# Optimization experiments

Measured on AMD Instinct MI355X. Metric: run time of the kernel, lower is better.

The kernel has to match this reference:

```python
import jax, jax.numpy as jnp
import numpy as np

N = 20000   # nodes per type per hop
E = 200000  # edges per relation per hop
H = 512     # node_feature_hid_len
FU = 512    # raw user feature len
FI = 256    # raw item feature len
NUM_RES = 2
NUM_DNN = 2


def setup_inputs() -> dict:
    key = jax.random.key(0)
    ks = iter(jax.random.split(key, 64))
    p = lambda shape: jax.random.normal(next(ks), shape, dtype=jnp.float32) * 0.05
    inp = {}
    # features per hop per type
    for h in range(3):
        inp[f'feat_user_h{h}'] = jax.random.normal(next(ks), (N, FU), dtype=jnp.float32)
        inp[f'feat_item_h{h}'] = jax.random.normal(next(ks), (N, FI), dtype=jnp.float32)
    del inp['feat_user_h2_']; 


def _unused():
    pass

# rebuild setup_inputs cleanly (above stub replaced)

def setup_inputs() -> dict:
    key = jax.random.key(0)
    ks = iter(jax.random.split(key, 64))
    p = lambda shape: jax.random.normal(next(ks), shape, dtype=jnp.float32) * 0.05
    inp = {}
    for h in range(3):
        inp[f'feat_user_h{h}'] = jax.random.normal(next(ks), (N, FU), dtype=jnp.float32)
        inp[f'feat_item_h{h}'] = jax.random.normal(next(ks), (N, FI), dtype=jnp.float32)
    for name in ('edges_UI_h0', 'edges_IU_h0', 'edges_UI_h1', 'edges_IU_h1'):
        inp[name] = jax.random.randint(next(ks), (2, E), 0, N, dtype=jnp.int32)
    # per-node-type input transforms
    inp['W_user'] = p((FU, H)); inp['b_user'] = jnp.zeros((H,), jnp.float32)
    inp['W_item'] = p((FI, H)); inp['b_item'] = jnp.zeros((H,), jnp.float32)
    # per-relation GATConv params, stacked over 2 relations [UI, IU]
    inp['gat_feat_W'] = p((2, H, H)); inp['gat_feat_b'] = jnp.zeros((2, H), jnp.float32)
    inp['gat_att_w'] = p((2, 2 * H)); inp['gat_att_b'] = jnp.zeros((2,), jnp.float32)
    inp['gat_bias'] = jnp.zeros((2, H), jnp.float32)
    # Res_DNN params
    inp['prep_W'] = p((H, H)); inp['prep_b'] = jnp.zeros((H,), jnp.float32)
    inp['dnn_W'] = p((NUM_RES, NUM_DNN, H, H)); inp['dnn_b'] = jnp.zeros((NUM_RES, NUM_DNN, H), jnp.float32)
    inp['dnn_ln_g'] = jnp.ones((NUM_RES, NUM_DNN, H), jnp.float32); inp['dnn_ln_b'] = jnp.zeros((NUM_RES, NUM_DNN, H), jnp.float32)
    inp['res_ln_g'] = jnp.ones((NUM_RES, H), jnp.float32); inp['res_ln_b'] = jnp.zeros((NUM_RES, H), jnp.float32)
    inp['cls_W'] = p((H, 1)); inp['cls_b'] = jnp.zeros((1,), jnp.float32)
    return inp


def _ln(x, g, b, eps=1e-5):
    mu = jnp.mean(x, axis=-1, keepdims=True)
    var = jnp.mean((x - mu) ** 2, axis=-1, keepdims=True)
    return (x - mu) * jax.lax.rsqrt(var + eps) * g + b


def _gat(head_h, tail_h, edges, fW, fb, aw, ab, bias):
    # GATConv: feat_linear on both sides, tanh edge attention, per-source-row
    # sparse softmax, scatter-weighted sum of transformed tail features.
    s = head_h @ fW + fb            # [Nh, H]
    t = tail_h @ fW + fb            # [Nt, H]
    src, tgt = edges[0], edges[1]
    # att(cat([s_e, t_e])) split into per-node scores (same math as concat @ aw)
    e = jnp.tanh((s @ aw[:H])[src] + (t @ aw[H:])[tgt] + ab)  # [E]
    nh = head_h.shape[0]
    m = jax.ops.segment_max(e, src, num_segments=nh)
    ex = jnp.exp(e - m[src])
    den = jax.ops.segment_sum(ex, src, num_segments=nh)
    alpha = ex / den[src]
    hp = jax.ops.segment_sum(alpha[:, None] * t[tgt], src, num_segments=nh)
    return hp + bias


def _forward(feat_user_h0, feat_item_h0, feat_user_h1, feat_item_h1,
             feat_user_h2, feat_item_h2,
             W_user, b_user, W_item, b_item,
             gat_feat_W, gat_feat_b, gat_att_w, gat_att_b, gat_bias,
             prep_W, prep_b, dnn_W, dnn_b, dnn_ln_g, dnn_ln_b,
             res_ln_g, res_ln_b, cls_W, cls_b,
             edges_UI_h0, edges_IU_h0, edges_UI_h1, edges_IU_h1):
    def gat(r, head, tail, edges):
        return _gat(head, tail, edges, gat_feat_W[r], gat_feat_b[r],
                    gat_att_w[r], gat_att_b[r], gat_bias[r])
    # hop 2 (deepest): transformed source features
    su = feat_user_h2 @ W_user + b_user
    si = feat_item_h2 @ W_item + b_item
    # hop 1
    hu = feat_user_h1 @ W_user + b_user
    hi = feat_item_h1 @ W_item + b_item
    su_new = (hu + gat(0, hu, si, edges_UI_h1)) * 0.5  # mean of [self, UI agg]
    si_new = (hi + gat(1, hi, su, edges_IU_h1)) * 0.5
    su, si = su_new, si_new
    # hop 0
    hu = feat_user_h0 @ W_user + b_user
    hi = feat_item_h0 @ W_item + b_item
    su_new = (hu + gat(0, hu, si, edges_UI_h0)) * 0.5
    su = su_new  # target node type = 'user' (first key)
    # Res_DNN head
    x = su @ prep_W + prep_b
    for r in range(NUM_RES):
        sc = x
        for d in range(NUM_DNN):
            x = _ln(jnp.tanh(x @ dnn_W[r, d] + dnn_b[r, d]), dnn_ln_g[r, d], dnn_ln_b[r, d])
        x = _ln(jnp.tanh(sc + x), res_ln_g[r], res_ln_b[r])
    return jax.nn.sigmoid(x @ cls_W + cls_b)  # [N, 1]


def reference(feat_user_h0, feat_item_h0, feat_user_h1, feat_item_h1,
              feat_user_h2, feat_item_h2,
              edges_UI_h0, edges_IU_h0, edges_UI_h1, edges_IU_h1,
              W_user, b_user, W_item, b_item,
              gat_feat_W, gat_feat_b, gat_att_w, gat_att_b, gat_bias,
              prep_W, prep_b, dnn_W, dnn_b, dnn_ln_g, dnn_ln_b,
              res_ln_g, res_ln_b, cls_W, cls_b):
    return _forward(feat_user_h0, feat_item_h0, feat_user_h1, feat_item_h1,
                    feat_user_h2, feat_item_h2,
                    W_user, b_user, W_item, b_item,
                    gat_feat_W, gat_feat_b, gat_att_w, gat_att_b, gat_bias,
                    prep_W, prep_b, dnn_W, dnn_b, dnn_ln_g, dnn_ln_b,
                    res_ln_g, res_ln_b, cls_W, cls_b,
                    edges_UI_h0, edges_IU_h0, edges_UI_h1, edges_IU_h1)
```

## Files before the change

### kernel.cpp

```cpp
#include <hip/hip_runtime.h>
#include <math.h>

#define NN 20000
#define NE 200000
#define HH 512

typedef __attribute__((ext_vector_type(8))) short short8v;
typedef __attribute__((ext_vector_type(4))) float f32x4;

__device__ inline short f2bf(float f) {
    union { float f; unsigned u; } v; v.f = f;
    unsigned r = (v.u + 0x7fffu + ((v.u >> 16) & 1u)) >> 16;
    return (short)r;
}
__device__ inline float bf2f(short s) {
    union { unsigned u; float f; } v;
    v.u = ((unsigned)(unsigned short)s) << 16;
    return v.f;
}

__device__ inline void gload_lds16(const void* g, void* l) {
    __builtin_amdgcn_global_load_lds(
        (const __attribute__((address_space(1))) void*)g,
        (__attribute__((address_space(3))) void*)l, 16, 0, 0);
}

__global__ __launch_bounds__(256)
void wtr_all(const float* __restrict__ Wu, const float* __restrict__ Wi,
             const float* __restrict__ gfW, const float* __restrict__ prW,
             const float* __restrict__ dW,
             short* __restrict__ WTu, short* __restrict__ WTi,
             short* __restrict__ WTg0, short* __restrict__ WTg1,
             short* __restrict__ WTpr, short* __restrict__ WTd)
{
    __shared__ float t[32][33];
    int z = blockIdx.z;
    const float* src; short* dst; int K;
    if (z == 0)      { src = Wu;  dst = WTu;  K = 512; }
    else if (z == 1) { src = Wi;  dst = WTi;  K = 256; }
    else if (z == 2) { src = gfW; dst = WTg0; K = 512; }
    else if (z == 3) { src = gfW + (size_t)512 * 512; dst = WTg1; K = 512; }
    else if (z == 4) { src = prW; dst = WTpr; K = 512; }
    else { src = dW + (size_t)(z - 5) * 512 * 512;
           dst = WTd + (size_t)(z - 5) * 512 * 512; K = 512; }
    int by = blockIdx.y * 32;
    if (by >= K) return;
    int bx = blockIdx.x * 32;
    int tx = threadIdx.x, ty = threadIdx.y;
    for (int i = ty; i < 32; i += 8)
        t[i][tx] = src[(size_t)(by + i) * 512 + bx + tx];
    __syncthreads();
    for (int i = ty; i < 32; i += 8)
        dst[(size_t)(bx + i) * K + by + tx] = f2bf(t[tx][i]);
}

__global__ __launch_bounds__(256)
void mfma_lin(const short* __restrict__ X, const short* __restrict__ WT,
              const float* __restrict__ bias, float* __restrict__ outF,
              short* __restrict__ outB, int M, int K,
              const short* __restrict__ rdH, const short* __restrict__ rdT,
              const float* __restrict__ rduv, const float* __restrict__ rds0,
              float* __restrict__ rdss, float* __restrict__ rdts, int rdN)
{
    __shared__ short8v pool[4096];

    const int tid = threadIdx.x;
    const int lane = tid & 63;
    const int w = tid >> 6;

    const int nby = (M + 127) >> 7;
    const int nwg = nby << 2;
    int id = blockIdx.x;

    if (id >= nwg) {
        int row = (id - nwg) * 4 + w;
        if (row >= rdN) return;
        short8v h = ((const short8v*)(rdH + (size_t)row * HH))[lane];
        short8v t = ((const short8v*)(rdT + (size_t)row * HH))[lane];
        const float4* up = (const float4*)rduv + lane * 2;
        const float4* vp = (const float4*)(rduv + HH) + lane * 2;
        float4 u0 = up[0], u1 = up[1], v0 = vp[0], v1 = vp[1];
        float a = bf2f(h[0])*u0.x + bf2f(h[1])*u0.y + bf2f(h[2])*u0.z + bf2f(h[3])*u0.w
                + bf2f(h[4])*u1.x + bf2f(h[5])*u1.y + bf2f(h[6])*u1.z + bf2f(h[7])*u1.w;
        float b = bf2f(t[0])*v0.x + bf2f(t[1])*v0.y + bf2f(t[2])*v0.z + bf2f(t[3])*v0.w
                + bf2f(t[4])*v1.x + bf2f(t[5])*v1.y + bf2f(t[6])*v1.z + bf2f(t[7])*v1.w;
#pragma unroll
        for (int m = 32; m >= 1; m >>= 1) {
            a += __shfl_xor(a, m);
            b += __shfl_xor(b, m);
        }
        if (lane == 0) { rdss[row] = a + rds0[0]; rdts[row] = b + rds0[1]; }
        return;
    }

    const int q = nwg >> 3, r = nwg & 7;
    int xcd = id & 7, wi = id >> 3;
    int wgid = (xcd < r ? xcd * (q + 1) : r * (q + 1) + (xcd - r) * q) + wi;
    const int col0 = (wgid & 3) * 128;
    const int row0 = (wgid >> 2) * 128;

    const int wr = (w >> 1) * 64;
    const int wc = (w & 1) * 64;

    const short* gsrc[8];
#pragma unroll
    for (int g = 0; g < 8; ++g) {
        int p = w * 512 + g * 64 + lane;
        if (p < 1024) {
            int row = p >> 3;
            int c = (p & 7) ^ (row & 7);
            int ga = row0 + row; if (ga >= M) ga = M - 1;
            gsrc[g] = X + (size_t)ga * K + c * 8;
        } else {
            int qq = p - 1024;
            int col = qq >> 3;
            int c = (qq & 7) ^ (col & 7);
            gsrc[g] = WT + (size_t)(col0 + col) * K + c * 8;
        }
    }

    int ar[2][4], br[2][4];
#pragma unroll
    for (int kk = 0; kk < 2; ++kk) {
#pragma unroll
        for (int i = 0; i < 4; ++i) {
            int rr = wr + i * 16 + (lane & 15);
            ar[kk][i] = rr * 8 + ((kk * 4 + (lane >> 4)) ^ (rr & 7));
            int nn = wc + i * 16 + (lane & 15);
            br[kk][i] = 1024 + nn * 8 + ((kk * 4 + (lane >> 4)) ^ (nn & 7));
        }
    }

    f32x4 acc[4][4];
#pragma unroll
    for (int i = 0; i < 4; ++i)
#pragma unroll
        for (int j = 0; j < 4; ++j)
            acc[i][j] = (f32x4){0.f, 0.f, 0.f, 0.f};

    auto stage = [&](int buf, int kk) {
        short8v* base = pool + buf * 2048 + w * 512;
#pragma unroll
        for (int g = 0; g < 8; ++g)
            gload_lds16(gsrc[g] + kk, base + g * 64);
    };

    const int nt = K >> 6;
    stage(0, 0);
    if (nt > 1) stage(1, 64);
    int cur = 0;
    for (int t = 0; t < nt; ++t) {
        if (t + 1 < nt) asm volatile("s_waitcnt vmcnt(8)" ::: "memory");
        else            asm volatile("s_waitcnt vmcnt(0)" ::: "memory");
        __builtin_amdgcn_s_barrier();
        const short8v* S = pool + cur * 2048;
#pragma unroll
        for (int kk = 0; kk < 2; ++kk) {
            short8v af[4], bf[4];
#pragma unroll
            for (int i = 0; i < 4; ++i) af[i] = S[ar[kk][i]];
#pragma unroll
            for (int j = 0; j < 4; ++j) bf[j] = S[br[kk][j]];
#pragma unroll
            for (int i = 0; i < 4; ++i)
#pragma unroll
                for (int j = 0; j < 4; ++j)
                    acc[i][j] = __builtin_amdgcn_mfma_f32_16x16x32_bf16(af[i], bf[j], acc[i][j], 0, 0, 0);
        }
        __builtin_amdgcn_s_barrier();
        if (t + 2 < nt) stage(cur, (t + 2) * 64);
        cur ^= 1;
    }

    float bj[4];
#pragma unroll
    for (int j = 0; j < 4; ++j)
        bj[j] = bias[col0 + wc + j * 16 + (lane & 15)];

    if (outF) {
#pragma unroll
        for (int i = 0; i < 4; ++i) {
#pragma unroll
            for (int rr = 0; rr < 4; ++rr) {
                int row = row0 + wr + i * 16 + (lane >> 4) * 4 + rr;
                if (row < M) {
                    float* op = outF + (size_t)row * HH + col0 + wc + (lane & 15);
#pragma unroll
                    for (int j = 0; j < 4; ++j) op[j * 16] = acc[i][j][rr] + bj[j];
                }
            }
        }
    }
    if (outB) {
        short* lt = (short*)pool;
#pragma unroll
        for (int i = 0; i < 4; ++i)
#pragma unroll
            for (int rr = 0; rr < 4; ++rr) {
                int lrow = wr + i * 16 + (lane >> 4) * 4 + rr;
#pragma unroll
                for (int j = 0; j < 4; ++j)
                    lt[lrow * 136 + wc + j * 16 + (lane & 15)] = f2bf(acc[i][j][rr] + bj[j]);
            }
        __syncthreads();
#pragma unroll
        for (int k = 0; k < 8; ++k) {
            int row = (tid >> 4) + 16 * k;
            int seg = tid & 15;
            int grow = row0 + row;
            if (grow < M) {
                short8v vv = *(short8v*)(lt + row * 136 + seg * 8);
                *(short8v*)(outB + (size_t)grow * HH + col0 + seg * 8) = vv;
            }
        }
    }
}

__global__ __launch_bounds__(256)
void mfma_linf(const float* __restrict__ XA, const float* __restrict__ XB2,
               int NA, const short* __restrict__ WT,
               const float* __restrict__ bias, short* __restrict__ outB,
               int M, int K)
{
    __shared__ short8v pool[3072];

    const int tid = threadIdx.x;
    const int lane = tid & 63;
    const int w = tid >> 6;

    const int nby = (M + 127) >> 7;
    const int nwg = nby << 2;
    const int q = nwg >> 3, r = nwg & 7;
    int id = blockIdx.x;
    int xcd = id & 7, wi = id >> 3;
    int wgid = (xcd < r ? xcd * (q + 1) : r * (q + 1) + (xcd - r) * q) + wi;
    const int col0 = (wgid & 3) * 128;
    const int row0 = (wgid >> 2) * 128;

    const int wr = (w >> 1) * 64;
    const int wc = (w & 1) * 64;
    const int kg = lane >> 4;

    const float* ga_[4];
#pragma unroll
    for (int g = 0; g < 4; ++g) {
        int p = w * 256 + g * 64 + lane;
        int row = p >> 3;
        int c = (p & 7) ^ (row & 7);
        int ga = row0 + row; if (ga >= M) ga = M - 1;
        const float* base = (ga < NA) ? XA + (size_t)ga * K
                                      : XB2 + (size_t)(ga - NA) * K;
        ga_[g] = base + c * 4;
    }
    const short* gb_[2];
#pragma unroll
    for (int g = 0; g < 2; ++g) {
        int p = w * 128 + g * 64 + lane;
        int col = p >> 2;
        int c = (p & 3) ^ ((col >> 1) & 3);
        gb_[g] = WT + (size_t)(col0 + col) * K + c * 8;
    }

    int arow[4], br_[4];
#pragma unroll
    for (int i = 0; i < 4; ++i) arow[i] = wr + i * 16 + (lane & 15);
#pragma unroll
    for (int j = 0; j < 4; ++j) {
        int nn = wc + j * 16 + (lane & 15);
        br_[j] = 1024 + nn * 4 + (kg ^ ((nn >> 1) & 3));
    }

    f32x4 acc[4][4];
#pragma unroll
    for (int i = 0; i < 4; ++i)
#pragma unroll
        for (int j = 0; j < 4; ++j)
            acc[i][j] = (f32x4){0.f, 0.f, 0.f, 0.f};

    auto stage = [&](int buf, int t) {
        short8v* base = pool + buf * 1536 + w * 256;
#pragma unroll
        for (int g = 0; g < 4; ++g)
            gload_lds16(ga_[g] + t * 32, base + g * 64);
        short8v* bb = pool + buf * 1536 + 1024 + w * 128;
#pragma unroll
        for (int g = 0; g < 2; ++g)
            gload_lds16(gb_[g] + t * 32, bb + g * 64);
    };

    const int nt = K >> 5;
    stage(0, 0);
    if (nt > 1) stage(1, 1);
    int cur = 0;
    for (int t = 0; t < nt; ++t) {
        if (t + 1 < nt) asm volatile("s_waitcnt vmcnt(6)" ::: "memory");
        else            asm volatile("s_waitcnt vmcnt(0)" ::: "memory");
        __builtin_amdgcn_s_barrier();
        const float4* Af = (const float4*)(pool + cur * 1536);
        const short8v* S = pool + cur * 1536;
        short8v af[4], bf[4];
#pragma unroll
        for (int i = 0; i < 4; ++i) {
            int rr = arow[i];
            int s = rr & 7;
            float4 lo = Af[rr * 8 + ((2 * kg)     ^ s)];
            float4 hi = Af[rr * 8 + ((2 * kg + 1) ^ s)];
            af[i][0] = f2bf(lo.x); af[i][1] = f2bf(lo.y);
            af[i][2] = f2bf(lo.z); af[i][3] = f2bf(lo.w);
            af[i][4] = f2bf(hi.x); af[i][5] = f2bf(hi.y);
            af[i][6] = f2bf(hi.z); af[i][7] = f2bf(hi.w);
        }
#pragma unroll
        for (int j = 0; j < 4; ++j) bf[j] = S[br_[j]];
#pragma unroll
        for (int i = 0; i < 4; ++i)
#pragma unroll
            for (int j = 0; j < 4; ++j)
                acc[i][j] = __builtin_amdgcn_mfma_f32_16x16x32_bf16(af[i], bf[j], acc[i][j], 0, 0, 0);
        __builtin_amdgcn_s_barrier();
        if (t + 2 < nt) stage(cur, t + 2);
        cur ^= 1;
    }

    float bj[4];
#pragma unroll
    for (int j = 0; j < 4; ++j)
        bj[j] = bias[col0 + wc + j * 16 + (lane & 15)];

    short* lt = (short*)pool;
#pragma unroll
    for (int i = 0; i < 4; ++i)
#pragma unroll
        for (int rr = 0; rr < 4; ++rr) {
            int lrow = wr + i * 16 + (lane >> 4) * 4 + rr;
#pragma unroll
            for (int j = 0; j < 4; ++j)
                lt[lrow * 136 + wc + j * 16 + (lane & 15)] = f2bf(acc[i][j][rr] + bj[j]);
        }
    __syncthreads();
#pragma unroll
    for (int k = 0; k < 8; ++k) {
        int row = (tid >> 4) + 16 * k;
        int seg = tid & 15;
        int grow = row0 + row;
        if (grow < M) {
            short8v vv = *(short8v*)(lt + row * 136 + seg * 8);
            *(short8v*)(outB + (size_t)grow * HH + col0 + seg * 8) = vv;
        }
    }
}

__global__ __launch_bounds__(256)
void gat_pre2(const float* __restrict__ gfW, const float* __restrict__ gfb,
              const float* __restrict__ gaw, float* __restrict__ uvall,
              float* __restrict__ s0t0all)
{
    int rrel = blockIdx.y;
    const float* fW = gfW + (size_t)rrel * HH * HH;
    const float* fb = gfb + rrel * HH;
    const float* aw = gaw + (size_t)rrel * 2 * HH;
    float* uv = uvall + rrel * 1024;
    float* s0t0 = s0t0all + rrel * 4;
    int row = blockIdx.x * 4 + (threadIdx.x >> 6);
    int lane = threadIdx.x & 63;
    const float4* ah = (const float4*)aw;
    const float4* at = (const float4*)(aw + HH);
    const float4* fp;
    if (row < 512)       fp = (const float4*)(fW + (size_t)row * HH);
    else if (row == 512) fp = (const float4*)fb;
    else return;
    float du = 0.f, dv = 0.f;
#pragma unroll
    for (int l = 0; l < 2; ++l) {
        int idx = lane * 2 + l;
        float4 f = fp[idx], a = ah[idx], b = at[idx];
        du += f.x*a.x + f.y*a.y + f.z*a.z + f.w*a.w;
        dv += f.x*b.x + f.y*b.y + f.z*b.z + f.w*b.w;
    }
#pragma unroll
    for (int m = 32; m >= 1; m >>= 1) {
        du += __shfl_xor(du, m);
        dv += __shfl_xor(dv, m);
    }
    if (lane == 0) {
        if (row < 512) { uv[row] = du; uv[512 + row] = dv; }
        else           { s0t0[0] = du; s0t0[1] = dv; }
    }
}

__global__ __launch_bounds__(256)
void count2_kernel(const int* __restrict__ s0, const int* __restrict__ s1,
                   int* __restrict__ c0, int* __restrict__ c1, int E)
{
    int i = blockIdx.x * blockDim.x + threadIdx.x;
    if (i < E) atomicAdd(&c0[s0[i]], 1);
    else if (i < 2 * E) atomicAdd(&c1[s1[i - E]], 1);
}

__global__ __launch_bounds__(1024)
void scan2_kernel(const int* __restrict__ c0, const int* __restrict__ c1,
                  int* __restrict__ o0, int* __restrict__ o1,
                  int* __restrict__ u0, int* __restrict__ u1, int n)
{
    const int* counts = blockIdx.x ? c1 : c0;
    int* offs = blockIdx.x ? o1 : o0;
    int* curs = blockIdx.x ? u1 : u0;
    __shared__ int part[1024];
    const int tid = threadIdx.x;
    const int CH = (n + 1023) / 1024;
    const int base = tid * CH;
    int s = 0;
    for (int i = 0; i < CH; ++i) {
        int idx = base + i;
        if (idx < n) s += counts[idx];
    }
    part[tid] = s;
    __syncthreads();
    for (int d = 1; d < 1024; d <<= 1) {
        int v = 0;
        if (tid >= d) v = part[tid - d];
        __syncthreads();
        if (tid >= d) part[tid] += v;
        __syncthreads();
    }
    int run = (tid == 0) ? 0 : part[tid - 1];
    for (int i = 0; i < CH; ++i) {
        int idx = base + i;
        if (idx < n) { offs[idx] = run; curs[idx] = run; run += counts[idx]; }
    }
    if (tid == 1023) offs[n] = run;
}

__global__ __launch_bounds__(256)
void fill_kernel(const int* __restrict__ src, const int* __restrict__ tgt,
                 const float* __restrict__ ss, const float* __restrict__ ts,
                 const float* __restrict__ ab_ptr, int* __restrict__ cursor,
                 int* __restrict__ tvals, float* __restrict__ wv,
                 int* __restrict__ eidx, int E)
{
    int i = blockIdx.x * blockDim.x + threadIdx.x;
    if (i >= E) return;
    int s = src[i], t = tgt[i];
    int pos = atomicAdd(&cursor[s], 1);
    tvals[pos] = t;
    wv[pos] = expf(tanhf(ss[s] + ts[t] + ab_ptr[0]));
    eidx[pos] = i;
}

__global__ __launch_bounds__(256)
void sortbkt_kernel(const int* __restrict__ offs, int* __restrict__ tvals,
                    float* __restrict__ wv, const int* __restrict__ eidx, int N)
{
    __shared__ int   lt[4][512];
    __shared__ float lw[4][512];
    int w = threadIdx.x >> 6, lane = threadIdx.x & 63;
    int s = blockIdx.x * 4 + w;
    if (s >= N) return;
    int beg = offs[s], end = offs[s + 1];
    int L = end - beg;
    if (L <= 1) return;
    if (L <= 64) {
        int e = 0x7fffffff, t = 0; float fw = 0.f;
        if (lane < L) { e = eidx[beg + lane]; t = tvals[beg + lane]; fw = wv[beg + lane]; }
        int r = 0;
        for (int k = 0; k < L; ++k) {
            int ek = __shfl(e, k);
            r += (ek < e) ? 1 : 0;
        }
        if (lane < L) { tvals[beg + r] = t; wv[beg + r] = fw; }
    } else if (L <= 512) {
        for (int j = lane; j < L; j += 64) { lt[w][j] = tvals[beg + j]; lw[w][j] = wv[beg + j]; }
        asm volatile("s_waitcnt lgkmcnt(0) vmcnt(0)" ::: "memory");
        for (int j = lane; j < L; j += 64) {
            int e = eidx[beg + j];
            int r = 0;
            for (int k = 0; k < L; ++k) r += (eidx[beg + k] < e) ? 1 : 0;
            tvals[beg + r] = lt[w][j]; wv[beg + r] = lw[w][j];
        }
    }
}

__global__ __launch_bounds__(256)
void gat_agg_kernel(const int* __restrict__ offs, const int* __restrict__ tvals,
                    const float* __restrict__ wv, const short* __restrict__ T,
                    const short* __restrict__ head, const float* __restrict__ gbias,
                    short* __restrict__ out, int N)
{
    int s = blockIdx.x * 4 + (threadIdx.x >> 6);
    int lane = threadIdx.x & 63;
    if (s >= N) return;
    const int beg = offs[s], end = offs[s + 1];
    float a[8];
#pragma unroll
    for (int q = 0; q < 8; ++q) a[q] = 0.f;
    float den = 0.f;

    int j = beg;
    for (; j + 4 <= end; j += 4) {
        int t0 = tvals[j], t1 = tvals[j + 1], t2 = tvals[j + 2], t3 = tvals[j + 3];
        float w0 = wv[j], w1 = wv[j + 1], w2 = wv[j + 2], w3 = wv[j + 3];
        short8v v0 = ((const short8v*)(T + (size_t)t0 * HH))[lane];
        short8v v1 = ((const short8v*)(T + (size_t)t1 * HH))[lane];
        short8v v2 = ((const short8v*)(T + (size_t)t2 * HH))[lane];
        short8v v3 = ((const short8v*)(T + (size_t)t3 * HH))[lane];
        den += w0 + w1 + w2 + w3;
#pragma unroll
        for (int q = 0; q < 8; ++q) {
            float acc = a[q];
            acc = fmaf(w0, bf2f(v0[q]), acc);
            acc = fmaf(w1, bf2f(v1[q]), acc);
            acc = fmaf(w2, bf2f(v2[q]), acc);
            acc = fmaf(w3, bf2f(v3[q]), acc);
            a[q] = acc;
        }
    }
    for (; j < end; ++j) {
        int t = tvals[j];
        float w = wv[j];
        short8v tv = ((const short8v*)(T + (size_t)t * HH))[lane];
        den += w;
#pragma unroll
        for (int q = 0; q < 8; ++q) a[q] = fmaf(w, bf2f(tv[q]), a[q]);
    }
    float inv = (den > 0.f) ? 1.f / den : 0.f;

    short8v h = ((const short8v*)(head + (size_t)s * HH))[lane];
    const float4* bp = (const float4*)gbias + lane * 2;
    float4 b0 = bp[0], b1 = bp[1];
    float bb[8] = {b0.x, b0.y, b0.z, b0.w, b1.x, b1.y, b1.z, b1.w};
    short8v o;
#pragma unroll
    for (int q = 0; q < 8; ++q)
        o[q] = f2bf((bf2f(h[q]) + a[q] * inv + bb[q]) * 0.5f);
    ((short8v*)(out + (size_t)s * HH))[lane] = o;
}

__global__ __launch_bounds__(256)
void tanh_ln_kernel(const short* __restrict__ Z,
                    const float* __restrict__ g, const float* __restrict__ bta,
                    short* __restrict__ outB, int N)
{
    int row = blockIdx.x * 4 + (threadIdx.x >> 6);
    int lane = threadIdx.x & 63;
    if (row >= N) return;
    short8v zv = ((const short8v*)(Z + (size_t)row * HH))[lane];
    float v[8];
    float sum = 0.f, sum2 = 0.f;
#pragma unroll
    for (int q = 0; q < 8; ++q) {
        float t = tanhf(bf2f(zv[q]));
        v[q] = t; sum += t; sum2 = fmaf(t, t, sum2);
    }
#pragma unroll
    for (int m = 32; m >= 1; m >>= 1) {
        sum += __shfl_xor(sum, m); sum2 += __shfl_xor(sum2, m);
    }
    float mu = sum * (1.f/HH);
    float rs = rsqrtf(sum2 * (1.f/HH) - mu*mu + 1e-5f);
    const float4* gp = (const float4*)g + lane * 2;
    const float4* bp = (const float4*)bta + lane * 2;
    float4 g0 = gp[0], g1 = gp[1], c0 = bp[0], c1 = bp[1];
    float gg[8] = {g0.x, g0.y, g0.z, g0.w, g1.x, g1.y, g1.z, g1.w};
    float cc[8] = {c0.x, c0.y, c0.z, c0.w, c1.x, c1.y, c1.z, c1.w};
    short8v ob;
#pragma unroll
    for (int q = 0; q < 8; ++q) ob[q] = f2bf((v[q]-mu)*rs*gg[q] + cc[q]);
    ((short8v*)(outB + (size_t)row * HH))[lane] = ob;
}

__global__ __launch_bounds__(256)
void tanh_ln2_kernel(const short* __restrict__ Z, const float* __restrict__ sc,
                     const float* __restrict__ g1, const float* __restrict__ b1,
                     const float* __restrict__ g2, const float* __restrict__ b2,
                     short* __restrict__ outB, float* __restrict__ outF,
                     const float* __restrict__ cWp, const float* __restrict__ cbp,
                     float* __restrict__ outCls, int N)
{
    int row = blockIdx.x * 4 + (threadIdx.x >> 6);
    int lane = threadIdx.x & 63;
    if (row >= N) return;
    short8v zv = ((const short8v*)(Z + (size_t)row * HH))[lane];
    float v[8];
    float sum = 0.f, sum2 = 0.f;
#pragma unroll
    for (int q = 0; q < 8; ++q) {
        float t = tanhf(bf2f(zv[q]));
        v[q] = t; sum += t; sum2 = fmaf(t, t, sum2);
    }
#pragma unroll
    for (int m = 32; m >= 1; m >>= 1) {
        sum += __shfl_xor(sum, m); sum2 += __shfl_xor(sum2, m);
    }
    float mu = sum * (1.f/HH);
    float rs = rsqrtf(sum2 * (1.f/HH) - mu*mu + 1e-5f);
    {
        const float4* gp = (const float4*)g1 + lane * 2;
        const float4* bp = (const float4*)b1 + lane * 2;
        float4 g0 = gp[0], g1v = gp[1], c0 = bp[0], c1 = bp[1];
        float gg[8] = {g0.x, g0.y, g0.z, g0.w, g1v.x, g1v.y, g1v.z, g1v.w};
        float cc[8] = {c0.x, c0.y, c0.z, c0.w, c1.x, c1.y, c1.z, c1.w};
        const float4* sp = (const float4*)(sc + (size_t)row * HH) + lane * 2;
        float4 s0 = sp[0], s1 = sp[1];
        float ssv[8] = {s0.x, s0.y, s0.z, s0.w, s1.x, s1.y, s1.z, s1.w};
        sum = 0.f; sum2 = 0.f;
#pragma unroll
        for (int q = 0; q < 8; ++q) {
            float x2 = (v[q]-mu)*rs*gg[q] + cc[q];
            float t = tanhf(ssv[q] + x2);
            v[q] = t; sum += t; sum2 = fmaf(t, t, sum2);
        }
    }
#pragma unroll
    for (int m = 32; m >= 1; m >>= 1) {
        sum += __shfl_xor(sum, m); sum2 += __shfl_xor(sum2, m);
    }
    mu = sum * (1.f/HH);
    rs = rsqrtf(sum2 * (1.f/HH) - mu*mu + 1e-5f);
    const float4* gp = (const float4*)g2 + lane * 2;
    const float4* bp = (const float4*)b2 + lane * 2;
    float4 g0 = gp[0], g1v = gp[1], c0 = bp[0], c1 = bp[1];
    float gg[8] = {g0.x, g0.y, g0.z, g0.w, g1v.x, g1v.y, g1v.z, g1v.w};
    float cc[8] = {c0.x, c0.y, c0.z, c0.w, c1.x, c1.y, c1.z, c1.w};
    float o[8];
#pragma unroll
    for (int q = 0; q < 8; ++q) o[q] = (v[q]-mu)*rs*gg[q] + cc[q];
    if (outB) {
        short8v ob;
#pragma unroll
        for (int q = 0; q < 8; ++q) ob[q] = f2bf(o[q]);
        ((short8v*)(outB + (size_t)row * HH))[lane] = ob;
    }
    if (outF) {
        float4* op = (float4*)(outF + (size_t)row * HH) + lane * 2;
        op[0] = make_float4(o[0], o[1], o[2], o[3]);
        op[1] = make_float4(o[4], o[5], o[6], o[7]);
    }
    if (cWp) {
        const float4* wp = (const float4*)cWp + lane * 2;
        float4 w0 = wp[0], w1 = wp[1];
        float acc = o[0]*w0.x + o[1]*w0.y + o[2]*w0.z + o[3]*w0.w
                  + o[4]*w1.x + o[5]*w1.y + o[6]*w1.z + o[7]*w1.w;
#pragma unroll
        for (int m = 32; m >= 1; m >>= 1) acc += __shfl_xor(acc, m);
        if (lane == 0) outCls[row] = 1.f / (1.f + expf(-(acc + cbp[0])));
    }
}

extern "C" void kernel_launch(void* const* d_in, const int* in_sizes, int n_in,
                              void* d_out, int out_size, void* d_ws, size_t ws_size,
                              hipStream_t stream)
{
    (void)in_sizes; (void)n_in; (void)out_size; (void)ws_size;
    const int N = NN, E = NE, H = HH;
    const size_t NHf = (size_t)N * H;

    const float* fu0 = (const float*)d_in[0];
    const float* fi1 = (const float*)d_in[3];
    const float* fu2 = (const float*)d_in[4];
    const int* eUI0 = (const int*)d_in[6];
    const int* eIU1 = (const int*)d_in[9];
    const float* Wu  = (const float*)d_in[10];
    const float* bu  = (const float*)d_in[11];
    const float* Wi  = (const float*)d_in[12];
    const float* bi  = (const float*)d_in[13];
    const float* gfW = (const float*)d_in[14];
    const float* gfb = (const float*)d_in[15];
    const float* gaw = (const float*)d_in[16];
    const float* gab = (const float*)d_in[17];
    const float* gbias = (const float*)d_in[18];
    const float* prW = (const float*)d_in[19];
    const float* prb = (const float*)d_in[20];
    const float* dW  = (const float*)d_in[21];
    const float* db  = (const float*)d_in[22];
    const float* dlg = (const float*)d_in[23];
    const float* dlb = (const float*)d_in[24];
    const float* rlg = (const float*)d_in[25];
    const float* rlb = (const float*)d_in[26];
    const float* cW  = (const float*)d_in[27];
    const float* cb  = (const float*)d_in[28];

    float* B5     = (float*)d_ws;
    float* ssb    = B5 + NHf;
    float* tsb    = ssb + N;
    float* uvall  = tsb + N;
    float* s0t0a  = uvall + 2048;
    float* wvb    = s0t0a + 8;
    int* counts0 = (int*)(wvb + E);
    int* counts1 = counts0 + N;
    int* offs0   = counts1 + N;
    int* offs1   = offs0 + N + 1;
    int* cur0    = offs1 + N + 1;
    int* cur1    = cur0 + N;
    int* tvals   = cur1 + N;
    int* eidxb   = tvals + E;
    size_t boff = (size_t)((char*)(eidxb + E) - (char*)d_ws);
    boff = (boff + 15) & ~(size_t)15;
    short* SUHU  = (short*)((char*)d_ws + boff);
    short* HI    = SUHU + 2 * NHf;
    short* SINEW = HI + NHf;
    short* T4    = SINEW + NHf;
    short* SUF   = T4 + NHf;
    short* WTu   = SUF + NHf;
    short* WTi   = WTu + 512 * 512;
    short* WTg0  = WTi + 512 * 256;
    short* WTg1  = WTg0 + 512 * 512;
    short* WTpr  = WTg1 + 512 * 512;
    short* WTd   = WTpr + 512 * 512;
    short* SU  = SUHU;
    short* HU0 = SUHU + NHf;
    short* XB  = SINEW;
    short* ZB  = SU;

    hipLaunchKernelGGL(wtr_all, dim3(16, 16, 9), dim3(32, 8), 0, stream,
                       Wu, Wi, gfW, prW, dW, WTu, WTi, WTg0, WTg1, WTpr, WTd);
    hipMemsetAsync(counts0, 0, 2 * N * sizeof(int), stream);
    hipLaunchKernelGGL(count2_kernel, dim3((2 * E + 255) / 256), dim3(256), 0, stream,
                       eUI0, eIU1, counts0, counts1, E);
    hipLaunchKernelGGL(scan2_kernel, dim3(2), dim3(1024), 0, stream,
                       counts0, counts1, offs0, offs1, cur0, cur1, N);
    hipLaunchKernelGGL(gat_pre2, dim3(130, 2), dim3(256), 0, stream,
                       gfW, gfb, gaw, uvall, s0t0a);

    const int rgrid = (N + 3) / 4;
    const int egrid = (E + 255) / 256;
    auto MLIN = [&](const short* X, const short* WT, const float* b,
                    float* oF, short* oB, int M, int K,
                    const short* rdH, const short* rdT, const float* rduv,
                    const float* rds0) {
        int nwg = ((M + 127) / 128) * 4;
        int grid = nwg + (rdH ? rgrid : 0);
        hipLaunchKernelGGL(mfma_lin, dim3(grid), dim3(256), 0, stream,
                           X, WT, b, oF, oB, M, K,
                           rdH, rdT, rduv, rds0, ssb, tsb, N);
    };
    auto MLINF = [&](const float* XA, const float* XB2, int NA, const short* WT,
                     const float* b, short* oB, int M, int K) {
        int nwg = ((M + 127) / 128) * 4;
        hipLaunchKernelGGL(mfma_linf, dim3(nwg), dim3(256), 0, stream,
                           XA, XB2, NA, WT, b, oB, M, K);
    };

    auto GAT = [&](int r, const short* headB, const short* tailB, const short* WTg,
                   const int* edges, int* offs, int* curs, short* outB) {
        MLIN(tailB, WTg, gfb + r * H, nullptr, T4, N, 512,
             headB, tailB, uvall + r * 1024, s0t0a + r * 4);
        hipLaunchKernelGGL(fill_kernel, dim3(egrid), dim3(256), 0, stream,
                           edges, edges + E, ssb, tsb, gab + r, curs, tvals, wvb,
                           eidxb, E);
        hipLaunchKernelGGL(sortbkt_kernel, dim3(rgrid), dim3(256), 0, stream,
                           offs, tvals, wvb, eidxb, N);
        hipLaunchKernelGGL(gat_agg_kernel, dim3(rgrid), dim3(256), 0, stream,
                           offs, tvals, wvb, T4, headB, gbias + (size_t)r * H, outB, N);
    };

    MLINF(fu2, fu0, N, WTu, bu, SUHU, 2 * N, 512);
    MLINF(fi1, fi1, N, WTi, bi, HI, N, 256);
    GAT(1, HI, SU, WTg1, eIU1, offs1, cur1, SINEW);
    GAT(0, HU0, SINEW, WTg0, eUI0, offs0, cur0, SUF);

    MLIN(SUF, WTpr, prb, B5, XB, N, 512, nullptr, nullptr, nullptr, nullptr);
    for (int r = 0; r < 2; ++r) {
        MLIN(XB, WTd + (size_t)(r * 2) * 512 * 512, db + (r * 2) * H,
             nullptr, ZB, N, 512, nullptr, nullptr, nullptr, nullptr);
        hipLaunchKernelGGL(tanh_ln_kernel, dim3(rgrid), dim3(256), 0, stream,
                           ZB, dlg + (r * 2) * H, dlb + (r * 2) * H, XB, N);
        MLIN(XB, WTd + (size_t)(r * 2 + 1) * 512 * 512, db + (r * 2 + 1) * H,
             nullptr, ZB, N, 512, nullptr, nullptr, nullptr, nullptr);
        if (r == 0) {
            hipLaunchKernelGGL(tanh_ln2_kernel, dim3(rgrid), dim3(256), 0, stream,
                               ZB, B5, dlg + H, dlb + H, rlg, rlb,
                               XB, B5, (const float*)nullptr, (const float*)nullptr,
                               (float*)nullptr, N);
        } else {
            hipLaunchKernelGGL(tanh_ln2_kernel, dim3(rgrid), dim3(256), 0, stream,
                               ZB, B5, dlg + 3 * H, dlb + 3 * H, rlg + H, rlb + H,
                               (short*)nullptr, (float*)nullptr, cW, cb,
                               (float*)d_out, N);
        }
    }
}
```

Measured before the change: 512.5 us.

## Convert fp32 A tile to bf16 in registers before LDS; unroll GAT gather by 8

The mfma_linf GEMM now loads fp32 A rows into registers, converts them to bf16 once per element, and writes a swizzled bf16 tile to LDS. Previously the raw fp32 tile went to LDS through global_load_lds and was converted at MFMA-operand time. This halves A-tile LDS footprint and LDS read traffic and removes repeated conversion work, at the cost of more registers and VGPR-routed loads. Separately, the GAT aggregation kernel gathers 8 neighbour rows per iteration to increase memory-level parallelism on the irregular gathers.

Result: no change. 506.1 us (-1.3%).

```diff
diff --git a/kernel.cpp b/kernel.cpp
--- a/kernel.cpp
+++ b/kernel.cpp
@@ -222,7 +222,7 @@
                const float* __restrict__ bias, short* __restrict__ outB,
                int M, int K)
 {
-    __shared__ short8v pool[3072];
+    __shared__ short8v pool[2304];
 
     const int tid = threadIdx.x;
     const int lane = tid & 63;
@@ -239,35 +239,38 @@
 
     const int wr = (w >> 1) * 64;
     const int wc = (w & 1) * 64;
-    const int kg = lane >> 4;
-
-    const float* ga_[4];
-#pragma unroll
-    for (int g = 0; g < 4; ++g) {
-        int p = w * 256 + g * 64 + lane;
-        int row = p >> 3;
-        int c = (p & 7) ^ (row & 7);
-        int ga = row0 + row; if (ga >= M) ga = M - 1;
-        const float* base = (ga < NA) ? XA + (size_t)ga * K
-                                      : XB2 + (size_t)(ga - NA) * K;
-        ga_[g] = base + c * 4;
-    }
-    const short* gb_[2];
-#pragma unroll
-    for (int g = 0; g < 2; ++g) {
-        int p = w * 128 + g * 64 + lane;
-        int col = p >> 2;
-        int c = (p & 3) ^ ((col >> 1) & 3);
-        gb_[g] = WT + (size_t)(col0 + col) * K + c * 8;
-    }
-
-    int arow[4], br_[4];
-#pragma unroll
-    for (int i = 0; i < 4; ++i) arow[i] = wr + i * 16 + (lane & 15);
-#pragma unroll
-    for (int j = 0; j < 4; ++j) {
-        int nn = wc + j * 16 + (lane & 15);
-        br_[j] = 1024 + nn * 4 + (kg ^ ((nn >> 1) & 3));
+
+    const int srow = tid >> 1;
+    const int sc0 = (tid & 1) * 2;
+    int garow = row0 + srow; if (garow >= M) garow = M - 1;
+    const float* abase = ((garow < NA) ? XA + (size_t)garow * K
+                                       : XB2 + (size_t)(garow - NA) * K) + sc0 * 8;
+    const int aswz = (srow >> 1) & 3;
+    const int wi0 = srow * 4 + (sc0 ^ aswz);
+    const int wi1 = srow * 4 + ((sc0 + 1) ^ aswz);
+
+    const short* bsrc0; const short* bsrc1;
+    int bbase0, bbase1;
+    {
+        int p0 = w * 128 + lane;
+        int col = p0 >> 2;
+        int c = (p0 & 3) ^ ((col >> 1) & 3);
+        bsrc0 = WT + (size_t)(col0 + col) * K + c * 8;
+        bbase0 = w * 128;
+        int p1 = w * 128 + 64 + lane;
+        col = p1 >> 2;
+        c = (p1 & 3) ^ ((col >> 1) & 3);
+        bsrc1 = WT + (size_t)(col0 + col) * K + c * 8;
+        bbase1 = w * 128 + 64;
+    }
+
+    int ar[4], br[4];
+#pragma unroll
+    for (int i = 0; i < 4; ++i) {
+        int rr = wr + i * 16 + (lane & 15);
+        ar[i] = rr * 4 + ((lane >> 4) ^ ((rr >> 1) & 3));
+        int nn = wc + i * 16 + (lane & 15);
+        br[i] = 512 + nn * 4 + ((lane >> 4) ^ ((nn >> 1) & 3));
     }
 
     f32x4 acc[4][4];
@@ -277,50 +280,52 @@
         for (int j = 0; j < 4; ++j)
             acc[i][j] = (f32x4){0.f, 0.f, 0.f, 0.f};
 
-    auto stage = [&](int buf, int t) {
-        short8v* base = pool + buf * 1536 + w * 256;
-#pragma unroll
-        for (int g = 0; g < 4; ++g)
-            gload_lds16(ga_[g] + t * 32, base + g * 64);
-        short8v* bb = pool + buf * 1536 + 1024 + w * 128;
-#pragma unroll
-        for (int g = 0; g < 2; ++g)
-            gload_lds16(gb_[g] + t * 32, bb + g * 64);
-    };
-
     const int nt = K >> 5;
-    stage(0, 0);
-    if (nt > 1) stage(1, 1);
-    int cur = 0;
-    for (int t = 0; t < nt; ++t) {
-        if (t + 1 < nt) asm volatile("s_waitcnt vmcnt(6)" ::: "memory");
-        else            asm volatile("s_waitcnt vmcnt(0)" ::: "memory");
-        __builtin_amdgcn_s_barrier();
-        const float4* Af = (const float4*)(pool + cur * 1536);
-        const short8v* S = pool + cur * 1536;
-        short8v af[4], bf[4];
-#pragma unroll
-        for (int i = 0; i < 4; ++i) {
-            int rr = arow[i];
-            int s = rr & 7;
-            float4 lo = Af[rr * 8 + ((2 * kg)     ^ s)];
-            float4 hi = Af[rr * 8 + ((2 * kg + 1) ^ s)];
-            af[i][0] = f2bf(lo.x); af[i][1] = f2bf(lo.y);
-            af[i][2] = f2bf(lo.z); af[i][3] = f2bf(lo.w);
-            af[i][4] = f2bf(hi.x); af[i][5] = f2bf(hi.y);
-            af[i][6] = f2bf(hi.z); af[i][7] = f2bf(hi.w);
-        }
-#pragma unroll
-        for (int j = 0; j < 4; ++j) bf[j] = S[br_[j]];
-#pragma unroll
-        for (int i = 0; i < 4; ++i)
-#pragma unroll
-            for (int j = 0; j < 4; ++j)
-                acc[i][j] = __builtin_amdgcn_mfma_f32_16x16x32_bf16(af[i], bf[j], acc[i][j], 0, 0, 0);
-        __builtin_amdgcn_s_barrier();
-        if (t + 2 < nt) stage(cur, t + 2);
-        cur ^= 1;
-    }
+    float4 rA0[4], rA1[4];
+
+#define ISSUE_A(RA, T) {                                                   \
+        const float4* p_ = (const float4*)(abase + (T) * 32);              \
+        RA[0] = p_[0]; RA[1] = p_[1]; RA[2] = p_[2]; RA[3] = p_[3]; }
+#define ISSUE_B(BUF, T) {                                                  \
+        short8v* bb_ = pool + (BUF) * 1024 + 512;                          \
+        gload_lds16(bsrc0 + (T) * 32, bb_ + bbase0);                       \
+        gload_lds16(bsrc1 + (T) * 32, bb_ + bbase1); }
+#define LINF_BODY(BUF, RA, T) {                                            \
+        short8v s0_, s1_;                                                  \
+        s0_[0]=f2bf(RA[0].x); s0_[1]=f2bf(RA[0].y); s0_[2]=f2bf(RA[0].z); s0_[3]=f2bf(RA[0].w); \
+        s0_[4]=f2bf(RA[1].x); s0_[5]=f2bf(RA[1].y); s0_[6]=f2bf(RA[1].z); s0_[7]=f2bf(RA[1].w); \
+        s1_[0]=f2bf(RA[2].x); s1_[1]=f2bf(RA[2].y); s1_[2]=f2bf(RA[2].z); s1_[3]=f2bf(RA[2].w); \
+        s1_[4]=f2bf(RA[3].x); s1_[5]=f2bf(RA[3].y); s1_[6]=f2bf(RA[3].z); s1_[7]=f2bf(RA[3].w); \
+        short8v* A_ = pool + (BUF) * 1024;                                 \
+        A_[wi0] = s0_; A_[wi1] = s1_;                                      \
+        if ((T) + 1 < nt) asm volatile("s_waitcnt vmcnt(6) lgkmcnt(0)" ::: "memory"); \
+        else              asm volatile("s_waitcnt vmcnt(0) lgkmcnt(0)" ::: "memory"); \
+        __builtin_amdgcn_s_barrier();                                      \
+        const short8v* S_ = pool + (BUF) * 1024;                           \
+        short8v af_[4], bf_[4];                                            \
+        _Pragma("unroll")                                                  \
+        for (int i_ = 0; i_ < 4; ++i_) af_[i_] = S_[ar[i_]];               \
+        _Pragma("unroll")                                                  \
+        for (int j_ = 0; j_ < 4; ++j_) bf_[j_] = S_[br[j_]];               \
+        _Pragma("unroll")                                                  \
+        for (int i_ = 0; i_ < 4; ++i_)                                     \
+            _Pragma("unroll")                                              \
+            for (int j_ = 0; j_ < 4; ++j_)                                 \
+                acc[i_][j_] = __builtin_amdgcn_mfma_f32_16x16x32_bf16(af_[i_], bf_[j_], acc[i_][j_], 0, 0, 0); \
+        __builtin_amdgcn_s_barrier();                                      \
+        if ((T) + 2 < nt) { ISSUE_A(RA, (T) + 2); ISSUE_B(BUF, (T) + 2); } }
+
+    ISSUE_A(rA0, 0);
+    ISSUE_B(0, 0);
+    ISSUE_A(rA1, 1);
+    ISSUE_B(1, 1);
+    for (int t = 0; t < nt; t += 2) {
+        LINF_BODY(0, rA0, t);
+        LINF_BODY(1, rA1, t + 1);
+    }
+#undef ISSUE_A
+#undef ISSUE_B
+#undef LINF_BODY
 
     float bj[4];
 #pragma unroll
@@ -496,22 +501,34 @@
     float den = 0.f;
 
     int j = beg;
+    for (; j + 8 <= end; j += 8) {
+        short8v v[8];
+        float wgt[8];
+#pragma unroll
+        for (int u = 0; u < 8; ++u) {
+            wgt[u] = wv[j + u];
+            v[u] = ((const short8v*)(T + (size_t)tvals[j + u] * HH))[lane];
+        }
+#pragma unroll
+        for (int u = 0; u < 8; ++u) {
+            den += wgt[u];
+#pragma unroll
+            for (int q = 0; q < 8; ++q) a[q] = fmaf(wgt[u], bf2f(v[u][q]), a[q]);
+        }
+    }
     for (; j + 4 <= end; j += 4) {
-        int t0 = tvals[j], t1 = tvals[j + 1], t2 = tvals[j + 2], t3 = tvals[j + 3];
-        float w0 = wv[j], w1 = wv[j + 1], w2 = wv[j + 2], w3 = wv[j + 3];
-        short8v v0 = ((const short8v*)(T + (size_t)t0 * HH))[lane];
-        short8v v1 = ((const short8v*)(T + (size_t)t1 * HH))[lane];
-        short8v v2 = ((const short8v*)(T + (size_t)t2 * HH))[lane];
-        short8v v3 = ((const short8v*)(T + (size_t)t3 * HH))[lane];
-        den += w0 + w1 + w2 + w3;
-#pragma unroll
-        for (int q = 0; q < 8; ++q) {
-            float acc = a[q];
-            acc = fmaf(w0, bf2f(v0[q]), acc);
-            acc = fmaf(w1, bf2f(v1[q]), acc);
-            acc = fmaf(w2, bf2f(v2[q]), acc);
-            acc = fmaf(w3, bf2f(v3[q]), acc);
-            a[q] = acc;
+        short8v v[4];
+        float wgt[4];
+#pragma unroll
+        for (int u = 0; u < 4; ++u) {
+            wgt[u] = wv[j + u];
+            v[u] = ((const short8v*)(T + (size_t)tvals[j + u] * HH))[lane];
+        }
+#pragma unroll
+        for (int u = 0; u < 4; ++u) {
+            den += wgt[u];
+#pragma unroll
+            for (int q = 0; q < 8; ++q) a[q] = fmaf(wgt[u], bf2f(v[u][q]), a[q]);
         }
     }
     for (; j < end; ++j) {
```
